# Kernel optimization log

Measured on AMD Instinct MI355X. Metric: run time of the kernel, lower is better.

Reference implementation:

```python
import jax, jax.numpy as jnp
import numpy as np
import math

VOCAB = 50000
EMB_DIM = 300
D_MODEL = 2048
BATCH = 4
SEQ = 8192


def setup_inputs() -> dict:
    key = jax.random.key(0)
    k1, k2, k3, k4 = jax.random.split(key, 4)
    x = jax.random.randint(k1, (BATCH, SEQ), 0, VOCAB, dtype=jnp.int64 if jax.config.jax_enable_x64 else jnp.int32)
    emb = jax.random.normal(k2, (VOCAB, EMB_DIM), dtype=jnp.float32)
    # nn.Linear(300, d_model): weight [d_model, 300] in torch; store transposed [300, d_model]
    W = jax.random.normal(k3, (EMB_DIM, D_MODEL), dtype=jnp.float32) * (1.0 / math.sqrt(EMB_DIM))
    b = jax.random.normal(k4, (D_MODEL,), dtype=jnp.float32) * 0.01
    return {"x": x, "emb": emb, "W": W, "b": b}


def reference(x, emb, W, b):
    # Dict lookup per token == single gather: [B, S] -> [B, S, 300]
    vecs = emb[x]
    # Linear(300 -> d_model) then scale by sqrt(d_model)
    out = jnp.einsum("bse,ed->bsd", vecs, W) + b
    return out * jnp.sqrt(jnp.asarray(W.shape[1], dtype=out.dtype))
```

## Files before the change

### kernel.cpp

```cpp
#include <hip/hip_runtime.h>


#define VOCAB 50000
#define TOKENS 32768
#define EMB 300
#define DM 2048
#define KPAD 320
#define SCALE 45.25483399593904f

typedef _Float16 f16;
typedef _Float16 h4 __attribute__((ext_vector_type(4)));
typedef _Float16 h8 __attribute__((ext_vector_type(8)));
typedef float f32x4 __attribute__((ext_vector_type(4)));

__device__ __forceinline__ void gload_lds16(const f16* g, f16* l) {
    __builtin_amdgcn_global_load_lds(
        (const __attribute__((address_space(1))) void*)g,
        (__attribute__((address_space(3))) void*)l, 16, 0, 0);
}

__global__ __launch_bounds__(256) void prep_emb(const float* __restrict__ emb,
                                                f16* __restrict__ embh) {
    int idx = blockIdx.x * 256 + threadIdx.x;
    if (idx >= VOCAB * 40) return;
    int row = idx / 40;
    int c = idx - row * 40;
    h8 hv = {};
    const float* src = emb + (size_t)row * EMB + (c << 3);
    if (c < 37) {
        float4 a = *(const float4*)src;
        float4 d = *(const float4*)(src + 4);
        hv[0]=(f16)a.x; hv[1]=(f16)a.y; hv[2]=(f16)a.z; hv[3]=(f16)a.w;
        hv[4]=(f16)d.x; hv[5]=(f16)d.y; hv[6]=(f16)d.z; hv[7]=(f16)d.w;
    } else if (c == 37) {
        float4 a = *(const float4*)src;
        hv[0]=(f16)a.x; hv[1]=(f16)a.y; hv[2]=(f16)a.z; hv[3]=(f16)a.w;
    }
    *(h8*)(embh + (size_t)row * KPAD + (c << 3)) = hv;
}

__global__ __launch_bounds__(256) void prep_wsw(const float* __restrict__ W,
                                                f16* __restrict__ Wsw) {
    int idx = blockIdx.x * 256 + threadIdx.x;
    int p = idx & 1023;
    int tile = idx >> 10;
    int kc = tile % 5;
    int ntile = tile / 5;
    int row = p >> 3, cpos = p & 7;
    int clog = cpos ^ (row & 7);
    int n = (ntile << 7) + row;
    int kbase = (kc << 6) + (clog << 3);
    h8 hv = {};
    #pragma unroll
    for (int j = 0; j < 8; ++j) {
        int k = kbase + j;
        if (k < EMB) hv[j] = (f16)W[(size_t)k * DM + n];
    }
    *(h8*)(Wsw + (size_t)idx * 8) = hv;
}

__global__ __launch_bounds__(256) void prep_b(const float* __restrict__ b, float* __restrict__ bs) {
    int i = blockIdx.x * 256 + threadIdx.x;
    if (i < DM) bs[i] = b[i] * SCALE;
}

__global__ __launch_bounds__(256, 4) void embed_gemm(
        const int* __restrict__ x, const f16* __restrict__ embh,
        const f16* __restrict__ Wsw, const float* __restrict__ bs,
        float* __restrict__ out)
{
    __shared__ __align__(16) f16 As[128 * 64];
    __shared__ __align__(16) f16 Bs[128 * 64];
    __shared__ int toks[128];

    const int lin  = blockIdx.x;
    const int xcd  = lin & 7;
    const int slot = lin >> 3;
    const int mtile = (xcd << 5) + (slot >> 4);
    const int ntile = slot & 15;
    const int m0 = mtile << 7;
    const int n0 = ntile << 7;

    const int t = threadIdx.x;
    const int lane = t & 63;
    const int wave = t >> 6;
    const int wm = (wave >> 1) << 6;
    const int wn = (wave & 1) << 6;
    const int quad = lane >> 4;
    const int lr = lane & 15;

    if (t < 128) toks[t] = x[m0 + t];
    __syncthreads();

    const int arow_lo = t >> 3;
    const int axor = ((t & 7) ^ (arow_lo & 7)) << 3;
    const f16* asrc[4];
    #pragma unroll
    for (int i = 0; i < 4; ++i)
        asrc[i] = embh + (size_t)toks[(i << 5) + arow_lo] * KPAD + axor;

    const f16* bsrc = Wsw + (size_t)ntile * 40960 + ((size_t)t << 3);

    f16* adst = As + (t << 3);
    f16* bdst = Bs + (t << 3);

    f32x4 acc[4][4] = {};

    for (int kc = 0; kc < 5; ++kc) {
        const int koff = kc << 6;
        #pragma unroll
        for (int i = 0; i < 4; ++i)
            gload_lds16(bsrc + (kc << 13) + (i << 11), bdst + (i << 11));
        #pragma unroll
        for (int i = 0; i < 4; ++i)
            gload_lds16(asrc[i] + koff, adst + (i << 11));
        __syncthreads();

        #pragma unroll
        for (int kk = 0; kk < 2; ++kk) {
            h8 af[4], bfr[4];
            const int c = (kk << 2) + quad;
            #pragma unroll
            for (int mi = 0; mi < 4; ++mi) {
                int m = wm + (mi << 4) + lr;
                af[mi] = *(const h8*)(As + (m << 6) + ((c ^ (m & 7)) << 3));
            }
            #pragma unroll
            for (int ni = 0; ni < 4; ++ni) {
                int n = wn + (ni << 4) + lr;
                bfr[ni] = *(const h8*)(Bs + (n << 6) + ((c ^ (n & 7)) << 3));
            }
            #pragma unroll
            for (int mi = 0; mi < 4; ++mi)
                #pragma unroll
                for (int ni = 0; ni < 4; ++ni)
                    acc[mi][ni] = __builtin_amdgcn_mfma_f32_16x16x32_f16(
                        af[mi], bfr[ni], acc[mi][ni], 0, 0, 0);
        }
        __syncthreads();
    }

    #pragma unroll
    for (int ni = 0; ni < 4; ++ni) {
        int n = n0 + wn + (ni << 4) + lr;
        float bias = bs[n];
        #pragma unroll
        for (int mi = 0; mi < 4; ++mi) {
            int mb = m0 + wm + (mi << 4) + (quad << 2);
            #pragma unroll
            for (int r = 0; r < 4; ++r) {
                out[(size_t)(mb + r) * DM + n] = fmaf(acc[mi][ni][r], SCALE, bias);
            }
        }
    }
}

__global__ __launch_bounds__(256) void prep_w_old(const float* __restrict__ W, f16* __restrict__ Wt) {
    __shared__ f16 tile[64 * 68];
    const int k0 = blockIdx.x << 6;
    const int n0 = blockIdx.y << 6;
    const int t = threadIdx.x;
    #pragma unroll
    for (int i = 0; i < 4; ++i) {
        int idx = (i << 8) + t;
        int kr = idx >> 4;
        int nc = idx & 15;
        h4 hv = {};
        if (k0 + kr < EMB) {
            float4 v = *(const float4*)(W + (size_t)(k0 + kr) * DM + n0 + (nc << 2));
            hv[0]=(f16)v.x; hv[1]=(f16)v.y; hv[2]=(f16)v.z; hv[3]=(f16)v.w;
        }
        *(h4*)(tile + kr * 68 + (nc << 2)) = hv;
    }
    __syncthreads();
    #pragma unroll
    for (int i = 0; i < 4; ++i) {
        int idx = (i << 8) + t;
        int n  = idx >> 4;
        int kc = idx & 15;
        h4 hv;
        hv[0] = tile[(kc * 4 + 0) * 68 + n];
        hv[1] = tile[(kc * 4 + 1) * 68 + n];
        hv[2] = tile[(kc * 4 + 2) * 68 + n];
        hv[3] = tile[(kc * 4 + 3) * 68 + n];
        *(h4*)(Wt + (size_t)(n0 + n) * KPAD + k0 + (kc << 2)) = hv;
    }
}

__global__ __launch_bounds__(256, 4) void embed_gemm_old(
        const int* __restrict__ x, const float* __restrict__ emb,
        const f16* __restrict__ Wt, const float* __restrict__ bs,
        float* __restrict__ out)
{
    __shared__ __align__(16) f16 As[128 * 64];
    __shared__ __align__(16) f16 Bs[128 * 64];
    __shared__ int toks[128];

    const int lin  = blockIdx.x;
    const int xcd  = lin & 7;
    const int slot = lin >> 3;
    const int mtile = (xcd << 5) + (slot >> 4);
    const int ntile = slot & 15;
    const int m0 = mtile << 7;
    const int n0 = ntile << 7;

    const int t = threadIdx.x;
    const int lane = t & 63;
    const int wave = t >> 6;
    const int wm = (wave >> 1) << 6;
    const int wn = (wave & 1) << 6;
    const int quad = lane >> 4;
    const int lr = lane & 15;

    if (t < 128) toks[t] = x[m0 + t];
    __syncthreads();

    f32x4 acc[4][4] = {};

    for (int kc = 0; kc < 5; ++kc) {
        const int k0 = kc << 6;
        #pragma unroll
        for (int i = 0; i < 4; ++i) {
            int idx = (i << 8) + t;
            int row = idx >> 3;
            int c   = idx & 7;
            h8 v = *(const h8*)(Wt + (size_t)(n0 + row) * KPAD + k0 + (c << 3));
            *(h8*)(Bs + (row << 6) + ((c ^ (row & 7)) << 3)) = v;
        }
        #pragma unroll
        for (int i = 0; i < 8; ++i) {
            int q   = (i << 8) + t;
            int row = q >> 4;
            int qc  = q & 15;
            int k   = k0 + (qc << 2);
            h4 hv = {};
            if (k + 3 < EMB) {
                float4 v = *(const float4*)(emb + (size_t)toks[row] * EMB + k);
                hv[0]=(f16)v.x; hv[1]=(f16)v.y; hv[2]=(f16)v.z; hv[3]=(f16)v.w;
            }
            int c = qc >> 1, half = qc & 1;
            *(h4*)(As + (row << 6) + (((c ^ (row & 7)) << 3) + (half << 2))) = hv;
        }
        __syncthreads();

        #pragma unroll
        for (int kk = 0; kk < 2; ++kk) {
            h8 af[4], bfr[4];
            const int c = (kk << 2) + quad;
            #pragma unroll
            for (int mi = 0; mi < 4; ++mi) {
                int m = wm + (mi << 4) + lr;
                af[mi] = *(const h8*)(As + (m << 6) + ((c ^ (m & 7)) << 3));
            }
            #pragma unroll
            for (int ni = 0; ni < 4; ++ni) {
                int n = wn + (ni << 4) + lr;
                bfr[ni] = *(const h8*)(Bs + (n << 6) + ((c ^ (n & 7)) << 3));
            }
            #pragma unroll
            for (int mi = 0; mi < 4; ++mi)
                #pragma unroll
                for (int ni = 0; ni < 4; ++ni)
                    acc[mi][ni] = __builtin_amdgcn_mfma_f32_16x16x32_f16(
                        af[mi], bfr[ni], acc[mi][ni], 0, 0, 0);
        }
        __syncthreads();
    }

    #pragma unroll
    for (int ni = 0; ni < 4; ++ni) {
        int n = n0 + wn + (ni << 4) + lr;
        float bias = bs[n];
        #pragma unroll
        for (int mi = 0; mi < 4; ++mi) {
            int mb = m0 + wm + (mi << 4) + (quad << 2);
            #pragma unroll
            for (int r = 0; r < 4; ++r) {
                out[(size_t)(mb + r) * DM + n] = fmaf(acc[mi][ni][r], SCALE, bias);
            }
        }
    }
}

__global__ __launch_bounds__(256) void naive_kernel(
        const int* __restrict__ x, const float* __restrict__ emb,
        const float* __restrict__ W, const float* __restrict__ b, float* __restrict__ out)
{
    size_t idx = (size_t)blockIdx.x * 256 + threadIdx.x;
    int n = (int)(idx & (DM - 1));
    size_t m = idx >> 11;
    const float* e = emb + (size_t)x[m] * EMB;
    float a = 0.f;
    for (int k = 0; k < EMB; ++k) a = fmaf(e[k], W[(size_t)k * DM + n], a);
    out[idx] = (a + b[n]) * SCALE;
}

extern "C" void kernel_launch(void* const* d_in, const int* in_sizes, int n_in,
                              void* d_out, int out_size, void* d_ws, size_t ws_size,
                              hipStream_t stream) {
    const int*   x   = (const int*)d_in[0];
    const float* emb = (const float*)d_in[1];
    const float* W   = (const float*)d_in[2];
    const float* b   = (const float*)d_in[3];
    float* out = (float*)d_out;

    const size_t embh_bytes = (size_t)VOCAB * KPAD * sizeof(f16);
    const size_t wsw_bytes  = (size_t)DM * KPAD * sizeof(f16);
    const size_t need_big   = embh_bytes + wsw_bytes + (size_t)DM * sizeof(float);
    const size_t need_small = wsw_bytes + (size_t)DM * sizeof(float);

    if (ws_size >= need_big) {
        f16* embh = (f16*)d_ws;
        f16* Wsw  = (f16*)((char*)d_ws + embh_bytes);
        float* bsp = (float*)((char*)d_ws + embh_bytes + wsw_bytes);
        prep_emb<<<(VOCAB * 40 + 255) / 256, 256, 0, stream>>>(emb, embh);
        prep_wsw<<<(16 * 5 * 1024) / 256, 256, 0, stream>>>(W, Wsw);
        prep_b<<<DM / 256, 256, 0, stream>>>(b, bsp);
        embed_gemm<<<(TOKENS / 128) * (DM / 128), 256, 0, stream>>>(x, embh, Wsw, bsp, out);
    } else if (ws_size >= need_small) {
        f16* Wt = (f16*)d_ws;
        float* bsp = (float*)((char*)d_ws + wsw_bytes);
        prep_w_old<<<dim3(KPAD / 64, DM / 64), 256, 0, stream>>>(W, Wt);
        prep_b<<<DM / 256, 256, 0, stream>>>(b, bsp);
        embed_gemm_old<<<(TOKENS / 128) * (DM / 128), 256, 0, stream>>>(x, emb, Wt, bsp, out);
    } else {
        naive_kernel<<<((size_t)TOKENS * DM) / 256, 256, 0, stream>>>(x, emb, W, b, out);
    }
}
```

Baseline: 393.7 us.

## Prepack W into MFMA fragment order, double-buffer A tiles, vectorize output stores

W is repacked into per-lane MFMA fragment order so each wave reads its B operands straight from global memory (L2-resident) instead of staging them through LDS. The A tile is now double-buffered in LDS, with the next K chunk prefetched while the current one is computed. The MFMA operand order is swapped so each lane holds four consecutive columns, which allows float4 bias loads and float4 output stores. This cuts LDS traffic and store instruction count, at the cost of global-load latency on the B operand inside the inner loop.

Result: slower. 408.8 us (+3.9%).

```diff
diff --git a/kernel.cpp b/kernel.cpp
--- a/kernel.cpp
+++ b/kernel.cpp
@@ -39,24 +39,29 @@
     *(h8*)(embh + (size_t)row * KPAD + (c << 3)) = hv;
 }
 
-__global__ __launch_bounds__(256) void prep_wsw(const float* __restrict__ W,
-                                                f16* __restrict__ Wsw) {
-    int idx = blockIdx.x * 256 + threadIdx.x;
-    int p = idx & 1023;
-    int tile = idx >> 10;
-    int kc = tile % 5;
-    int ntile = tile / 5;
-    int row = p >> 3, cpos = p & 7;
-    int clog = cpos ^ (row & 7);
-    int n = (ntile << 7) + row;
-    int kbase = (kc << 6) + (clog << 3);
+__global__ __launch_bounds__(256) void prep_wfrag(const float* __restrict__ W,
+                                                  f16* __restrict__ Wf) {
+    int g = blockIdx.x * 256 + threadIdx.x;
+    int lane = g & 63;
+    int blk = g >> 6;
+    int ni = blk & 3;
+    int kk = (blk >> 2) & 1;
+    int rest = blk >> 3;
+    int kc = rest % 5;
+    int whnt = rest / 5;
+    int wh = whnt & 1;
+    int ntile = whnt >> 1;
+    int lr = lane & 15, quad = lane >> 4;
+    int n = (ntile << 7) + (wh << 6) + (ni << 4) + lr;
+    int kbase = (kc << 6) + ((kk << 2) + quad) << 3 ? 0 : 0;
+    kbase = (kc << 6) + (((kk << 2) + quad) << 3);
     h8 hv = {};
     #pragma unroll
     for (int j = 0; j < 8; ++j) {
         int k = kbase + j;
         if (k < EMB) hv[j] = (f16)W[(size_t)k * DM + n];
     }
-    *(h8*)(Wsw + (size_t)idx * 8) = hv;
+    *(h8*)(Wf + (size_t)g * 8) = hv;
 }
 
 __global__ __launch_bounds__(256) void prep_b(const float* __restrict__ b, float* __restrict__ bs) {
@@ -66,11 +71,10 @@
 
 __global__ __launch_bounds__(256, 4) void embed_gemm(
         const int* __restrict__ x, const f16* __restrict__ embh,
-        const f16* __restrict__ Wsw, const float* __restrict__ bs,
+        const f16* __restrict__ Wf, const float* __restrict__ bs,
         float* __restrict__ out)
 {
-    __shared__ __align__(16) f16 As[128 * 64];
-    __shared__ __align__(16) f16 Bs[128 * 64];
+    __shared__ __align__(16) f16 As[2][128 * 64];
     __shared__ int toks[128];
 
     const int lin  = blockIdx.x;
@@ -94,63 +98,72 @@
 
     const int arow_lo = t >> 3;
     const int axor = ((t & 7) ^ (arow_lo & 7)) << 3;
-    const f16* asrc[4];
+    unsigned aoff[4];
     #pragma unroll
     for (int i = 0; i < 4; ++i)
-        asrc[i] = embh + (size_t)toks[(i << 5) + arow_lo] * KPAD + axor;
-
-    const f16* bsrc = Wsw + (size_t)ntile * 40960 + ((size_t)t << 3);
-
-    f16* adst = As + (t << 3);
-    f16* bdst = Bs + (t << 3);
+        aoff[i] = (unsigned)toks[(i << 5) + arow_lo] * KPAD + axor;
+
+    const f16* wfb = Wf + (size_t)((ntile << 1) + (wave & 1)) * 20480;
+
+    f16* adst = &As[0][0] + (t << 3);
+
+    #pragma unroll
+    for (int i = 0; i < 4; ++i)
+        gload_lds16(embh + aoff[i], adst + (i << 11));
+    __syncthreads();
 
     f32x4 acc[4][4] = {};
 
     for (int kc = 0; kc < 5; ++kc) {
-        const int koff = kc << 6;
-        #pragma unroll
-        for (int i = 0; i < 4; ++i)
-            gload_lds16(bsrc + (kc << 13) + (i << 11), bdst + (i << 11));
-        #pragma unroll
-        for (int i = 0; i < 4; ++i)
-            gload_lds16(asrc[i] + koff, adst + (i << 11));
-        __syncthreads();
-
+        if (kc < 4) {
+            f16* ad = &As[(kc + 1) & 1][0] + (t << 3);
+            const int koff = (kc + 1) << 6;
+            #pragma unroll
+            for (int i = 0; i < 4; ++i)
+                gload_lds16(embh + aoff[i] + koff, ad + (i << 11));
+        }
+
+        const f16* ab = &As[kc & 1][0];
         #pragma unroll
         for (int kk = 0; kk < 2; ++kk) {
-            h8 af[4], bfr[4];
+            h8 bfr[4];
+            const int fb = ((kc << 1) + kk) << 2;
+            #pragma unroll
+            for (int ni = 0; ni < 4; ++ni)
+                bfr[ni] = *(const h8*)(wfb + ((fb + ni) << 9) + (lane << 3));
+            h8 af[4];
             const int c = (kk << 2) + quad;
             #pragma unroll
             for (int mi = 0; mi < 4; ++mi) {
                 int m = wm + (mi << 4) + lr;
-                af[mi] = *(const h8*)(As + (m << 6) + ((c ^ (m & 7)) << 3));
-            }
-            #pragma unroll
-            for (int ni = 0; ni < 4; ++ni) {
-                int n = wn + (ni << 4) + lr;
-                bfr[ni] = *(const h8*)(Bs + (n << 6) + ((c ^ (n & 7)) << 3));
+                af[mi] = *(const h8*)(ab + (m << 6) + ((c ^ (m & 7)) << 3));
             }
             #pragma unroll
             for (int mi = 0; mi < 4; ++mi)
                 #pragma unroll
                 for (int ni = 0; ni < 4; ++ni)
                     acc[mi][ni] = __builtin_amdgcn_mfma_f32_16x16x32_f16(
-                        af[mi], bfr[ni], acc[mi][ni], 0, 0, 0);
+                        bfr[ni], af[mi], acc[mi][ni], 0, 0, 0);
         }
         __syncthreads();
     }
 
-    #pragma unroll
-    for (int ni = 0; ni < 4; ++ni) {
-        int n = n0 + wn + (ni << 4) + lr;
-        float bias = bs[n];
-        #pragma unroll
-        for (int mi = 0; mi < 4; ++mi) {
-            int mb = m0 + wm + (mi << 4) + (quad << 2);
-            #pragma unroll
-            for (int r = 0; r < 4; ++r) {
-                out[(size_t)(mb + r) * DM + n] = fmaf(acc[mi][ni][r], SCALE, bias);
-            }
+    float4 b4[4];
+    #pragma unroll
+    for (int ni = 0; ni < 4; ++ni)
+        b4[ni] = *(const float4*)(bs + n0 + wn + (ni << 4) + (quad << 2));
+    #pragma unroll
+    for (int mi = 0; mi < 4; ++mi) {
+        const int m = m0 + wm + (mi << 4) + lr;
+        float* orow = out + (size_t)m * DM + n0 + wn + (quad << 2);
+        #pragma unroll
+        for (int ni = 0; ni < 4; ++ni) {
+            float4 v;
+            v.x = fmaf(acc[mi][ni][0], SCALE, b4[ni].x);
+            v.y = fmaf(acc[mi][ni][1], SCALE, b4[ni].y);
+            v.z = fmaf(acc[mi][ni][2], SCALE, b4[ni].z);
+            v.w = fmaf(acc[mi][ni][3], SCALE, b4[ni].w);
+            *(float4*)(orow + (ni << 4)) = v;
         }
     }
 }
@@ -192,8 +205,8 @@
         const f16* __restrict__ Wt, const float* __restrict__ bs,
         float* __restrict__ out)
 {
-    __shared__ __align__(16) f16 As[128 * 64];
-    __shared__ __align__(16) f16 Bs[128 * 64];
+    __shared__ __align__(16) f16 Asl[128 * 64];
+    __shared__ __align__(16) f16 Bsl[128 * 64];
     __shared__ int toks[128];
 
     const int lin  = blockIdx.x;
@@ -225,7 +238,7 @@
             int row = idx >> 3;
             int c   = idx & 7;
             h8 v = *(const h8*)(Wt + (size_t)(n0 + row) * KPAD + k0 + (c << 3));
-            *(h8*)(Bs + (row << 6) + ((c ^ (row & 7)) << 3)) = v;
+            *(h8*)(Bsl + (row << 6) + ((c ^ (row & 7)) << 3)) = v;
         }
         #pragma unroll
         for (int i = 0; i < 8; ++i) {
@@ -239,7 +252,7 @@
                 hv[0]=(f16)v.x; hv[1]=(f16)v.y; hv[2]=(f16)v.z; hv[3]=(f16)v.w;
             }
             int c = qc >> 1, half = qc & 1;
-            *(h4*)(As + (row << 6) + (((c ^ (row & 7)) << 3) + (half << 2))) = hv;
+            *(h4*)(Asl + (row << 6) + (((c ^ (row & 7)) << 3) + (half << 2))) = hv;
         }
         __syncthreads();
 
@@ -250,12 +263,12 @@
             #pragma unroll
             for (int mi = 0; mi < 4; ++mi) {
                 int m = wm + (mi << 4) + lr;
-                af[mi] = *(const h8*)(As + (m << 6) + ((c ^ (m & 7)) << 3));
+                af[mi] = *(const h8*)(Asl + (m << 6) + ((c ^ (m & 7)) << 3));
             }
             #pragma unroll
             for (int ni = 0; ni < 4; ++ni) {
                 int n = wn + (ni << 4) + lr;
-                bfr[ni] = *(const h8*)(Bs + (n << 6) + ((c ^ (n & 7)) << 3));
+                bfr[ni] = *(const h8*)(Bsl + (n << 6) + ((c ^ (n & 7)) << 3));
             }
             #pragma unroll
             for (int mi = 0; mi < 4; ++mi)
@@ -305,21 +318,21 @@
     float* out = (float*)d_out;
 
     const size_t embh_bytes = (size_t)VOCAB * KPAD * sizeof(f16);
-    const size_t wsw_bytes  = (size_t)DM * KPAD * sizeof(f16);
-    const size_t need_big   = embh_bytes + wsw_bytes + (size_t)DM * sizeof(float);
-    const size_t need_small = wsw_bytes + (size_t)DM * sizeof(float);
+    const size_t wf_bytes   = (size_t)DM * KPAD * sizeof(f16);
+    const size_t need_big   = embh_bytes + wf_bytes + (size_t)DM * sizeof(float);
+    const size_t need_small = wf_bytes + (size_t)DM * sizeof(float);
 
     if (ws_size >= need_big) {
         f16* embh = (f16*)d_ws;
-        f16* Wsw  = (f16*)((char*)d_ws + embh_bytes);
-        float* bsp = (float*)((char*)d_ws + embh_bytes + wsw_bytes);
+        f16* Wf   = (f16*)((char*)d_ws + embh_bytes);
+        float* bsp = (float*)((char*)d_ws + embh_bytes + wf_bytes);
         prep_emb<<<(VOCAB * 40 + 255) / 256, 256, 0, stream>>>(emb, embh);
-        prep_wsw<<<(16 * 5 * 1024) / 256, 256, 0, stream>>>(W, Wsw);
+        prep_wfrag<<<(16 * 5 * 1024) / 256, 256, 0, stream>>>(W, Wf);
         prep_b<<<DM / 256, 256, 0, stream>>>(b, bsp);
-        embed_gemm<<<(TOKENS / 128) * (DM / 128), 256, 0, stream>>>(x, embh, Wsw, bsp, out);
+        embed_gemm<<<(TOKENS / 128) * (DM / 128), 256, 0, stream>>>(x, embh, Wf, bsp, out);
     } else if (ws_size >= need_small) {
         f16* Wt = (f16*)d_ws;
-        float* bsp = (float*)((char*)d_ws + wsw_bytes);
+        float* bsp = (float*)((char*)d_ws + wf_bytes);
         prep_w_old<<<dim3(KPAD / 64, DM / 64), 256, 0, stream>>>(W, Wt);
         prep_b<<<DM / 256, 256, 0, stream>>>(b, bsp);
         embed_gemm_old<<<(TOKENS / 128) * (DM / 128), 256, 0, stream>>>(x, emb, Wt, bsp, out);
```
